# Kernel optimization log

Measured on AMD Instinct MI355X. Metric: run time of the kernel, lower is better.

The kernel has to match this reference:

```python
import jax, jax.numpy as jnp
import numpy as np

N_NODES = 50000
N_EDGES = 800000
IN_F = 256
OUT_F = 64


def setup_inputs() -> dict:
    key = jax.random.key(0)
    k1, k2, k3, k4, k5 = jax.random.split(key, 5)
    x = jax.random.normal(k1, (N_NODES, IN_F), dtype=jnp.float32)
    # xavier-uniform-like init for weight
    limit = float(np.sqrt(6.0 / (IN_F + OUT_F)))
    weight = jax.random.uniform(k2, (IN_F, OUT_F), dtype=jnp.float32, minval=-limit, maxval=limit)
    bias = jnp.zeros((1, OUT_F), dtype=jnp.float32)
    edge_weight = jax.random.uniform(k3, (N_EDGES,), dtype=jnp.float32)
    edge_src = jax.random.randint(k4, (N_EDGES,), 0, N_NODES, dtype=jnp.int32)
    edge_dst = jax.random.randint(k5, (N_EDGES,), 0, N_NODES, dtype=jnp.int32)
    return {"x": x, "weight": weight, "bias": bias,
            "edge_weight": edge_weight, "edge_src": edge_src, "edge_dst": edge_dst}


def reference(x, weight, bias, edge_weight, edge_src, edge_dst):
    # in_features (256) > out_features (64): transform first, then propagate.
    h = x @ weight                                  # [N, out]
    # spmm with COO adjacency: out[dst] += w_e * h[src]
    msgs = h[edge_src] * edge_weight[:, None]       # [E, out]
    out = jax.ops.segment_sum(msgs, edge_dst, num_segments=x.shape[0])  # [N, out]
    return out + bias
```

## Files before the change

### kernel.cpp

```cpp
#include <hip/hip_runtime.h>
#include <hip/hip_bf16.h>

#define N_NODES 50000
#define N_EDGES 800000
#define IN_F 256
#define OUT_F 64

#define CAP 64

typedef __attribute__((ext_vector_type(8))) short short8;
typedef __attribute__((ext_vector_type(4))) float f32x4;

static __device__ __forceinline__ ushort f2bf(float v) {
    __hip_bfloat16 b = __float2bfloat16(v);
    return *(ushort*)&b;
}

__global__ __launch_bounds__(256) void gc_prep(const float* __restrict__ W,
                                               ushort* __restrict__ Wb,
                                               int* __restrict__ cnt) {
    const int g = blockIdx.x * 256 + threadIdx.x;
    if (g < N_NODES) cnt[g] = 0;
    if (g < 2048) {
        const int s = g >> 9;
        const int kk = (g >> 6) & 7;
        const int lane = g & 63;
        const int n = s * 16 + (lane & 15);
        const int kb = kk * 32 + (lane >> 4) * 8;
#pragma unroll
        for (int j = 0; j < 8; ++j)
            Wb[(size_t)g * 8 + j] = f2bf(W[(kb + j) * OUT_F + n]);
    }
}

__global__ __launch_bounds__(256) void gc_place(const int* __restrict__ esrc,
                                                const int* __restrict__ edst,
                                                const float* __restrict__ ew,
                                                int* __restrict__ cnt,
                                                unsigned int* __restrict__ slots) {
    const int e = blockIdx.x * 1024 + threadIdx.x * 4;
    if (e < N_EDGES) {
        const int4 s4 = *(const int4*)(esrc + e);
        const int4 d4 = *(const int4*)(edst + e);
        const float4 w4 = *(const float4*)(ew + e);

        const int p0 = atomicAdd(&cnt[d4.x], 1);
        const int p1 = atomicAdd(&cnt[d4.y], 1);
        const int p2 = atomicAdd(&cnt[d4.z], 1);
        const int p3 = atomicAdd(&cnt[d4.w], 1);

        if (p0 < CAP)
            slots[(size_t)d4.x * CAP + p0] =
                ((unsigned)f2bf(w4.x) << 16) | (unsigned)(s4.x & 0xFFFF);
        if (p1 < CAP)
            slots[(size_t)d4.y * CAP + p1] =
                ((unsigned)f2bf(w4.y) << 16) | (unsigned)(s4.y & 0xFFFF);
        if (p2 < CAP)
            slots[(size_t)d4.z * CAP + p2] =
                ((unsigned)f2bf(w4.z) << 16) | (unsigned)(s4.z & 0xFFFF);
        if (p3 < CAP)
            slots[(size_t)d4.w * CAP + p3] =
                ((unsigned)f2bf(w4.w) << 16) | (unsigned)(s4.w & 0xFFFF);
    }
}

__global__ __launch_bounds__(256) void gc_gemm(const float* __restrict__ x,
                                               const ushort* __restrict__ Wb,
                                               ushort* __restrict__ h) {
    __shared__ ushort xs[32 * 264];
    const int t = threadIdx.x;
    const int nbase = blockIdx.x * 32;

    {
#pragma unroll
        for (int i = 0; i < 8; ++i) {
            const int idx = t + i * 256;
            const int node = idx >> 6;
            const int c4 = idx & 63;
            int gnode = nbase + node;
            if (gnode >= N_NODES) gnode = N_NODES - 1;
            const float4 v = ((const float4*)x)[(size_t)gnode * 64 + c4];
            ushort4 b;
            b.x = f2bf(v.x); b.y = f2bf(v.y); b.z = f2bf(v.z); b.w = f2bf(v.w);
            *(ushort4*)&xs[node * 264 + c4 * 4] = b;
        }
    }

    const int s = t >> 6;
    const int lane = t & 63;
    const int m = lane & 15;
    const int quad = lane >> 4;

    short8 bfrag[8];
#pragma unroll
    for (int kk = 0; kk < 8; ++kk)
        bfrag[kk] = *(const short8*)(Wb + ((size_t)(s * 8 + kk) * 64 + lane) * 8);

    __syncthreads();

    f32x4 acc0 = {0.f, 0.f, 0.f, 0.f};
    f32x4 acc1 = {0.f, 0.f, 0.f, 0.f};
#pragma unroll
    for (int kk = 0; kk < 8; ++kk) {
        const short8 a0 = *(const short8*)&xs[m * 264 + kk * 32 + quad * 8];
        const short8 a1 = *(const short8*)&xs[(16 + m) * 264 + kk * 32 + quad * 8];
        acc0 = __builtin_amdgcn_mfma_f32_16x16x32_bf16(a0, bfrag[kk], acc0, 0, 0, 0);
        acc1 = __builtin_amdgcn_mfma_f32_16x16x32_bf16(a1, bfrag[kk], acc1, 0, 0, 0);
    }

#pragma unroll
    for (int r = 0; r < 4; ++r) {
        const int row0 = nbase + quad * 4 + r;
        const int row1 = row0 + 16;
        if (row0 < N_NODES) h[(size_t)row0 * OUT_F + s * 16 + m] = f2bf(acc0[r]);
        if (row1 < N_NODES) h[(size_t)row1 * OUT_F + s * 16 + m] = f2bf(acc1[r]);
    }
}

__global__ __launch_bounds__(256) void gc_gather(const ushort* __restrict__ h,
                                                 const unsigned int* __restrict__ slots,
                                                 const int* __restrict__ cnt,
                                                 const float* __restrict__ bias,
                                                 float* __restrict__ out) {
    const int wid = __builtin_amdgcn_readfirstlane(
        (int)((blockIdx.x * 256 + threadIdx.x) >> 6));
    const int f = threadIdx.x & 63;
    const int d0 = wid * 8;
    if (d0 >= N_NODES) return;

    const int4 ca = *(const int4*)(cnt + d0);
    const int4 cb = *(const int4*)(cnt + d0 + 4);
    const int dg0 = min(ca.x, CAP), dg1 = min(ca.y, CAP);
    const int dg2 = min(ca.z, CAP), dg3 = min(ca.w, CAP);
    const int dg4 = min(cb.x, CAP), dg5 = min(cb.y, CAP);
    const int dg6 = min(cb.z, CAP), dg7 = min(cb.w, CAP);
    const int mdeg = max(max(max(dg0, dg1), max(dg2, dg3)),
                         max(max(dg4, dg5), max(dg6, dg7)));

    const unsigned sw0 = (f < dg0) ? slots[(size_t)(d0 + 0) * CAP + f] : 0u;
    const unsigned sw1 = (f < dg1) ? slots[(size_t)(d0 + 1) * CAP + f] : 0u;
    const unsigned sw2 = (f < dg2) ? slots[(size_t)(d0 + 2) * CAP + f] : 0u;
    const unsigned sw3 = (f < dg3) ? slots[(size_t)(d0 + 3) * CAP + f] : 0u;
    const unsigned sw4 = (f < dg4) ? slots[(size_t)(d0 + 4) * CAP + f] : 0u;
    const unsigned sw5 = (f < dg5) ? slots[(size_t)(d0 + 5) * CAP + f] : 0u;
    const unsigned sw6 = (f < dg6) ? slots[(size_t)(d0 + 6) * CAP + f] : 0u;
    const unsigned sw7 = (f < dg7) ? slots[(size_t)(d0 + 7) * CAP + f] : 0u;

    const float b = bias[f];
    float a0 = b, a1 = b, a2 = b, a3 = b, a4 = b, a5 = b, a6 = b, a7 = b;

    const ushort* __restrict__ hf = h + f;

#define ROWLD(sw, l) \
    hf[(size_t)((unsigned)__builtin_amdgcn_readlane((int)(sw), (l)) & 0xFFFFu) * OUT_F]
#define WBITS(sw, l) \
    __uint_as_float((unsigned)__builtin_amdgcn_readlane((int)(sw), (l)) & 0xFFFF0000u)

    for (int i0 = 0; i0 < mdeg; i0 += 8) {
        unsigned hv0[8], hv1[8], hv2[8], hv3[8], hv4[8], hv5[8], hv6[8], hv7[8];
#pragma unroll
        for (int j = 0; j < 8; ++j) {
            const int l = i0 + j;
            hv0[j] = ROWLD(sw0, l);
            hv1[j] = ROWLD(sw1, l);
            hv2[j] = ROWLD(sw2, l);
            hv3[j] = ROWLD(sw3, l);
            hv4[j] = ROWLD(sw4, l);
            hv5[j] = ROWLD(sw5, l);
            hv6[j] = ROWLD(sw6, l);
            hv7[j] = ROWLD(sw7, l);
        }
#pragma unroll
        for (int j = 0; j < 8; ++j) {
            const int l = i0 + j;
            a0 += WBITS(sw0, l) * __uint_as_float(hv0[j] << 16);
            a1 += WBITS(sw1, l) * __uint_as_float(hv1[j] << 16);
            a2 += WBITS(sw2, l) * __uint_as_float(hv2[j] << 16);
            a3 += WBITS(sw3, l) * __uint_as_float(hv3[j] << 16);
            a4 += WBITS(sw4, l) * __uint_as_float(hv4[j] << 16);
            a5 += WBITS(sw5, l) * __uint_as_float(hv5[j] << 16);
            a6 += WBITS(sw6, l) * __uint_as_float(hv6[j] << 16);
            a7 += WBITS(sw7, l) * __uint_as_float(hv7[j] << 16);
        }
    }
#undef ROWLD
#undef WBITS

    out[(size_t)(d0 + 0) * OUT_F + f] = a0;
    out[(size_t)(d0 + 1) * OUT_F + f] = a1;
    out[(size_t)(d0 + 2) * OUT_F + f] = a2;
    out[(size_t)(d0 + 3) * OUT_F + f] = a3;
    out[(size_t)(d0 + 4) * OUT_F + f] = a4;
    out[(size_t)(d0 + 5) * OUT_F + f] = a5;
    out[(size_t)(d0 + 6) * OUT_F + f] = a6;
    out[(size_t)(d0 + 7) * OUT_F + f] = a7;
}

extern "C" void kernel_launch(void* const* d_in, const int* in_sizes, int n_in,
                              void* d_out, int out_size, void* d_ws, size_t ws_size,
                              hipStream_t stream) {
    const float* x    = (const float*)d_in[0];
    const float* W    = (const float*)d_in[1];
    const float* bias = (const float*)d_in[2];
    const float* ew   = (const float*)d_in[3];
    const int* src    = (const int*)d_in[4];
    const int* dst    = (const int*)d_in[5];
    float* out = (float*)d_out;

    char* ws = (char*)d_ws;
    ushort* h           = (ushort*)ws;
    int* cnt            = (int*)(ws + 6400000);
    unsigned int* slots = (unsigned int*)(ws + 6600000);
    ushort* Wb          = (ushort*)(ws + 19400000);

    gc_prep<<<196, 256, 0, stream>>>(W, Wb, cnt);
    gc_place<<<782, 256, 0, stream>>>(src, dst, ew, cnt, slots);
    gc_gemm<<<1563, 256, 0, stream>>>(x, Wb, h);
    gc_gather<<<1563, 256, 0, stream>>>(h, slots, cnt, bias, out);
}
```

Before: 170.8 us.

## Pre-bucket edges by destination range before slot placement to localize atomics

Adds a bucketing pass that partitions edges into 16 destination-range buckets using a shared-memory histogram and one global cursor atomic per bucket per block. A second pass then does the per-destination atomicAdd and slot writes bucket by bucket, so the counters and slot rows each block touches fall within a narrower address range. The aim is better cache locality for the scattered atomics and slot stores. The cost is an extra kernel launch plus writing and re-reading an 8-byte-per-edge arena that reuses the h buffer region.

```diff
diff --git a/kernel.cpp b/kernel.cpp
--- a/kernel.cpp
+++ b/kernel.cpp
@@ -7,6 +7,8 @@
 #define OUT_F 64
 
 #define CAP 64
+#define NBKT 16
+#define BKT_CAP 51200
 
 typedef __attribute__((ext_vector_type(8))) short short8;
 typedef __attribute__((ext_vector_type(4))) float f32x4;
@@ -15,12 +17,17 @@
     __hip_bfloat16 b = __float2bfloat16(v);
     return *(ushort*)&b;
 }
+static __device__ __forceinline__ int bkt_of(int dst) {
+    return (int)(((unsigned long long)(unsigned)dst * 1374390ull) >> 32);
+}
 
 __global__ __launch_bounds__(256) void gc_prep(const float* __restrict__ W,
                                                ushort* __restrict__ Wb,
-                                               int* __restrict__ cnt) {
+                                               int* __restrict__ cnt,
+                                               int* __restrict__ cursor) {
     const int g = blockIdx.x * 256 + threadIdx.x;
     if (g < N_NODES) cnt[g] = 0;
+    if (g < NBKT) cursor[g] = 0;
     if (g < 2048) {
         const int s = g >> 9;
         const int kk = (g >> 6) & 7;
@@ -33,34 +40,68 @@
     }
 }
 
-__global__ __launch_bounds__(256) void gc_place(const int* __restrict__ esrc,
-                                                const int* __restrict__ edst,
-                                                const float* __restrict__ ew,
-                                                int* __restrict__ cnt,
-                                                unsigned int* __restrict__ slots) {
-    const int e = blockIdx.x * 1024 + threadIdx.x * 4;
-    if (e < N_EDGES) {
+__global__ __launch_bounds__(256) void gc_bucket(const int* __restrict__ esrc,
+                                                 const int* __restrict__ edst,
+                                                 const float* __restrict__ ew,
+                                                 int* __restrict__ cursor,
+                                                 uint2* __restrict__ arena) {
+    __shared__ int hist[NBKT];
+    __shared__ int base[NBKT];
+    const int t = threadIdx.x;
+    if (t < NBKT) hist[t] = 0;
+    __syncthreads();
+
+    const int e = blockIdx.x * 1024 + t * 4;
+    const bool valid = e < N_EDGES;
+    int b[4], loff[4];
+    uint2 ent[4];
+    if (valid) {
         const int4 s4 = *(const int4*)(esrc + e);
         const int4 d4 = *(const int4*)(edst + e);
         const float4 w4 = *(const float4*)(ew + e);
-
-        const int p0 = atomicAdd(&cnt[d4.x], 1);
-        const int p1 = atomicAdd(&cnt[d4.y], 1);
-        const int p2 = atomicAdd(&cnt[d4.z], 1);
-        const int p3 = atomicAdd(&cnt[d4.w], 1);
-
-        if (p0 < CAP)
-            slots[(size_t)d4.x * CAP + p0] =
-                ((unsigned)f2bf(w4.x) << 16) | (unsigned)(s4.x & 0xFFFF);
-        if (p1 < CAP)
-            slots[(size_t)d4.y * CAP + p1] =
-                ((unsigned)f2bf(w4.y) << 16) | (unsigned)(s4.y & 0xFFFF);
-        if (p2 < CAP)
-            slots[(size_t)d4.z * CAP + p2] =
-                ((unsigned)f2bf(w4.z) << 16) | (unsigned)(s4.z & 0xFFFF);
-        if (p3 < CAP)
-            slots[(size_t)d4.w * CAP + p3] =
-                ((unsigned)f2bf(w4.w) << 16) | (unsigned)(s4.w & 0xFFFF);
+        const int ds[4] = {d4.x, d4.y, d4.z, d4.w};
+        const int ss[4] = {s4.x, s4.y, s4.z, s4.w};
+        const float wf[4] = {w4.x, w4.y, w4.z, w4.w};
+#pragma unroll
+        for (int j = 0; j < 4; ++j) {
+            b[j] = bkt_of(ds[j]);
+            ent[j].x = (unsigned)ds[j];
+            ent[j].y = ((unsigned)f2bf(wf[j]) << 16) | (unsigned)(ss[j] & 0xFFFF);
+            loff[j] = atomicAdd(&hist[b[j]], 1);
+        }
+    }
+    __syncthreads();
+    if (t < NBKT) base[t] = atomicAdd(&cursor[t], hist[t]);
+    __syncthreads();
+    if (valid) {
+#pragma unroll
+        for (int j = 0; j < 4; ++j)
+            arena[(size_t)b[j] * BKT_CAP + base[b[j]] + loff[j]] = ent[j];
+    }
+}
+
+__global__ __launch_bounds__(256) void gc_place2(const uint2* __restrict__ arena,
+                                                 const int* __restrict__ cursor,
+                                                 int* __restrict__ cnt,
+                                                 unsigned int* __restrict__ slots) {
+    const int b = blockIdx.x & (NBKT - 1);
+    const int j = blockIdx.x >> 4;
+    const int n = cursor[b];
+    const int i = j * 1024 + threadIdx.x * 4;
+    if (i >= n) return;
+
+    const uint2* __restrict__ p = arena + (size_t)b * BKT_CAP + i;
+    const uint4 e01 = *(const uint4*)p;
+    const uint4 e23 = *(const uint4*)(p + 2);
+
+    const unsigned dd[4] = {e01.x, e01.z, e23.x, e23.z};
+    const unsigned sw[4] = {e01.y, e01.w, e23.y, e23.w};
+#pragma unroll
+    for (int k = 0; k < 4; ++k) {
+        if (i + k < n) {
+            const int pos = atomicAdd(&cnt[dd[k]], 1);
+            if (pos < CAP) slots[(size_t)dd[k] * CAP + pos] = sw[k];
+        }
     }
 }
 
@@ -80,9 +121,9 @@
             int gnode = nbase + node;
             if (gnode >= N_NODES) gnode = N_NODES - 1;
             const float4 v = ((const float4*)x)[(size_t)gnode * 64 + c4];
-            ushort4 b;
-            b.x = f2bf(v.x); b.y = f2bf(v.y); b.z = f2bf(v.z); b.w = f2bf(v.w);
-            *(ushort4*)&xs[node * 264 + c4 * 4] = b;
+            ushort4 bv;
+            bv.x = f2bf(v.x); bv.y = f2bf(v.y); bv.z = f2bf(v.z); bv.w = f2bf(v.w);
+            *(ushort4*)&xs[node * 264 + c4 * 4] = bv;
         }
     }
 
@@ -208,13 +249,16 @@
     float* out = (float*)d_out;
 
     char* ws = (char*)d_ws;
+    uint2* arena        = (uint2*)ws;
     ushort* h           = (ushort*)ws;
-    int* cnt            = (int*)(ws + 6400000);
-    unsigned int* slots = (unsigned int*)(ws + 6600000);
-    ushort* Wb          = (ushort*)(ws + 19400000);
-
-    gc_prep<<<196, 256, 0, stream>>>(W, Wb, cnt);
-    gc_place<<<782, 256, 0, stream>>>(src, dst, ew, cnt, slots);
+    int* cnt            = (int*)(ws + 6553600);
+    unsigned int* slots = (unsigned int*)(ws + 6753600);
+    ushort* Wb          = (ushort*)(ws + 19553600);
+    int* cursor         = (int*)(ws + 19586368);
+
+    gc_prep<<<196, 256, 0, stream>>>(W, Wb, cnt, cursor);
+    gc_bucket<<<782, 256, 0, stream>>>(src, dst, ew, cursor, arena);
+    gc_place2<<<1024, 256, 0, stream>>>(arena, cursor, cnt, slots);
     gc_gemm<<<1563, 256, 0, stream>>>(x, Wb, h);
     gc_gather<<<1563, 256, 0, stream>>>(h, slots, cnt, bias, out);
 }
```

New measurement: 168.7 us. About the same (-1.2%).
